# Kernel tuning notes

Measured on AMD Instinct MI355X. Metric: run time of the kernel, lower is better.

The kernel has to match this reference:

```python
import jax, jax.numpy as jnp
import numpy as np

N_NODES = 100000
N_EDGES = 1600000
D_IN = 128
D_HID = 128
D_OUT = 1


def setup_inputs() -> dict:
    key = jax.random.key(0)
    ks = jax.random.split(key, 8)
    x = jax.random.normal(ks[0], (N_NODES, D_IN), dtype=jnp.float32)
    edge_index = jax.random.randint(ks[1], (2, N_EDGES), 0, N_NODES, dtype=jnp.int64)
    s1 = 1.0 / np.sqrt(D_IN)
    s2 = 1.0 / np.sqrt(D_HID)
    W1 = jax.random.uniform(ks[2], (D_IN, D_HID), jnp.float32, -s1, s1)
    b1 = jnp.zeros((D_HID,), jnp.float32)
    W2 = jax.random.uniform(ks[3], (D_HID, D_HID), jnp.float32, -s2, s2)
    b2 = jnp.zeros((D_HID,), jnp.float32)
    Wl = jax.random.uniform(ks[4], (D_HID, D_OUT), jnp.float32, -s2, s2)
    bl = jax.random.uniform(ks[5], (D_OUT,), jnp.float32, -s2, s2)
    return {"x": x, "edge_index": edge_index, "W1": W1, "b1": b1,
            "W2": W2, "b2": b2, "Wl": Wl, "bl": bl}


def _gcn_norm(edge_index, num_nodes):
    # Add self-loops, compute symmetric normalization 1/sqrt(deg_s * deg_d).
    loops = jnp.arange(num_nodes, dtype=edge_index.dtype)
    src = jnp.concatenate([edge_index[0], loops])
    dst = jnp.concatenate([edge_index[1], loops])
    deg = jax.ops.segment_sum(jnp.ones_like(dst, dtype=jnp.float32), dst,
                              num_segments=num_nodes)
    dinv = jnp.where(deg > 0, jax.lax.rsqrt(deg), 0.0)
    norm = dinv[src] * dinv[dst]  # [E + N]
    return src, dst, norm


def _gcn_conv(h, W, b, src, dst, norm, num_nodes):
    h = h @ W                                  # [N, d_out]
    msg = h[src] * norm[:, None]               # [E+N, d_out] gather
    out = jax.ops.segment_sum(msg, dst, num_segments=num_nodes)  # scatter-add
    return out + b


def reference(x, edge_index, W1, b1, W2, b2, Wl, bl):
    num_nodes = x.shape[0]
    src, dst, norm = _gcn_norm(edge_index, num_nodes)
    h = jax.nn.relu(_gcn_conv(x, W1, b1, src, dst, norm, num_nodes))
    # dropout is identity in eval mode
    h = jax.nn.relu(_gcn_conv(h, W2, b2, src, dst, norm, num_nodes))
    return h @ Wl + bl
```

## Files before the change

kernel.cpp:

```cpp
#include <hip/hip_runtime.h>

#define DHID 128
#define BCAP 10240
#define PCHUNK 4096
#define XS_LD 136
#define SMEM_BYTES 21504

typedef _Float16 h4 __attribute__((ext_vector_type(4)));
typedef _Float16 h8 __attribute__((ext_vector_type(8)));
typedef float    f32x4 __attribute__((ext_vector_type(4)));

__device__ inline void hoist_afrag_f16(const _Float16* __restrict__ Wt, int w, int l16, int lq,
                                       h8 afrag[2][4]) {
#pragma unroll
    for (int ct = 0; ct < 2; ++ct) {
        int c = w * 32 + ct * 16 + l16;
#pragma unroll
        for (int kb = 0; kb < 4; ++kb)
            afrag[ct][kb] = *(const h8*)(Wt + (size_t)c * DHID + kb * 32 + lq * 8);
    }
}

__global__ __launch_bounds__(256) void k_prep(const float* __restrict__ W1,
                                              const float* __restrict__ W2,
                                              _Float16* __restrict__ W1t,
                                              _Float16* __restrict__ W2t) {
    const float* W = (blockIdx.x == 0) ? W1 : W2;
    _Float16* Wt   = (blockIdx.x == 0) ? W1t : W2t;
    int t = threadIdx.x;
    int c = t & 127, k0 = (t >> 7) * 64;
#pragma unroll
    for (int kb = 0; kb < 8; ++kb) {
        h8 v;
#pragma unroll
        for (int j = 0; j < 8; ++j)
            v[j] = (_Float16)W[(size_t)(k0 + kb * 8 + j) * DHID + c];
        *(h8*)(Wt + (size_t)c * DHID + k0 + kb * 8) = v;
    }
}

__device__ inline void gemm1_body(char* smem, const float* __restrict__ X,
                                  const _Float16* __restrict__ W1t,
                                  _Float16* __restrict__ Th, int N, int blk) {
    _Float16* Xs = (_Float16*)smem;
    int t = threadIdx.x;
    int w = t >> 6, l = t & 63, l16 = l & 15, lq = l >> 4;

    h8 afrag[2][4];
    hoist_afrag_f16(W1t, w, l16, lq, afrag);

    int rs = t >> 2, cs = (t & 3) * 32;
    int r0 = blk * 64;
    {
        int rg = r0 + rs; if (rg > N - 1) rg = N - 1;
        _Float16* sp = Xs + rs * XS_LD + cs;
        const float* xp = X + (size_t)rg * DHID + cs;
#pragma unroll
        for (int k = 0; k < 4; ++k) {
            float4 a = *(const float4*)(xp + k * 8);
            float4 b = *(const float4*)(xp + k * 8 + 4);
            h8 v;
            v[0] = (_Float16)a.x; v[1] = (_Float16)a.y;
            v[2] = (_Float16)a.z; v[3] = (_Float16)a.w;
            v[4] = (_Float16)b.x; v[5] = (_Float16)b.y;
            v[6] = (_Float16)b.z; v[7] = (_Float16)b.w;
            *(h8*)(sp + k * 8) = v;
        }
    }
    __syncthreads();

    f32x4 acc[4][2];
#pragma unroll
    for (int rt = 0; rt < 4; ++rt)
#pragma unroll
        for (int ct = 0; ct < 2; ++ct) acc[rt][ct] = (f32x4){0.f, 0.f, 0.f, 0.f};

#pragma unroll
    for (int rt = 0; rt < 4; ++rt) {
        const _Float16* bp = Xs + (rt * 16 + l16) * XS_LD + lq * 8;
#pragma unroll
        for (int kb = 0; kb < 4; ++kb) {
            h8 b = *(const h8*)(bp + kb * 32);
            acc[rt][0] = __builtin_amdgcn_mfma_f32_16x16x32_f16(afrag[0][kb], b, acc[rt][0], 0, 0, 0);
            acc[rt][1] = __builtin_amdgcn_mfma_f32_16x16x32_f16(afrag[1][kb], b, acc[rt][1], 0, 0, 0);
        }
    }

#pragma unroll
    for (int rt = 0; rt < 4; ++rt) {
        int r = r0 + rt * 16 + l16;
        if (r < N) {
#pragma unroll
            for (int ct = 0; ct < 2; ++ct) {
                h4 v;
#pragma unroll
                for (int j = 0; j < 4; ++j) v[j] = (_Float16)acc[rt][ct][j];
                *(h4*)(Th + (size_t)r * DHID + w * 32 + ct * 16 + lq * 4) = v;
            }
        }
    }
}

__device__ inline void partition_body(char* smem, const int* __restrict__ ei, int E, int nbuck,
                                      int* __restrict__ bcur, unsigned* __restrict__ packed, int blk) {
    unsigned* sdata = (unsigned*)smem;
    int* lcnt  = (int*)(smem + 16384);
    int* lbase = (int*)(smem + 17408);
    int* loff  = (int*)(smem + 18432);
    int* lcur  = (int*)(smem + 19456);
    int* sscan = (int*)(smem + 20480);
    int t = threadIdx.x;
    int e0 = blk * PCHUNK;
    lcnt[t] = 0;
    __syncthreads();

    int sreg[16], dreg[16];
#pragma unroll
    for (int k = 0; k < 16; ++k) {
        int e = e0 + t + k * 256;
        if (e < E) { sreg[k] = ei[e]; dreg[k] = ei[E + e]; }
        else dreg[k] = -1;
    }

#pragma unroll
    for (int k = 0; k < 16; ++k)
        if (dreg[k] >= 0) atomicAdd(&lcnt[dreg[k] >> 9], 1);
    __syncthreads();

    int c = lcnt[t];
    sscan[t] = c;
    __syncthreads();
    for (int off = 1; off < 256; off <<= 1) {
        int v = (t >= off) ? sscan[t - off] : 0;
        __syncthreads();
        sscan[t] += v;
        __syncthreads();
    }
    loff[t] = sscan[t] - c;
    if (t < nbuck && c > 0) lbase[t] = atomicAdd(&bcur[t], c);
    lcur[t] = sscan[t] - c;
    __syncthreads();

#pragma unroll
    for (int k = 0; k < 16; ++k) {
        if (dreg[k] >= 0) {
            int b = dreg[k] >> 9;
            int pos = atomicAdd(&lcur[b], 1);
            sdata[pos] = ((unsigned)(dreg[k] & 511) << 17) | (unsigned)sreg[k];
        }
    }
    __syncthreads();

    int wid = t >> 6, lane = t & 63;
    for (int b = wid; b < nbuck; b += 4) {
        int cb = lcnt[b];
        if (cb == 0) continue;
        int gbase = b * BCAP + lbase[b];
        int sbase = loff[b];
        for (int k = lane; k < cb; k += 64) packed[gbase + k] = sdata[sbase + k];
    }
}

__global__ __launch_bounds__(256) void k_front(const float* __restrict__ X,
                                               const _Float16* __restrict__ W1t,
                                               _Float16* __restrict__ Th, int N, int nRB,
                                               const int* __restrict__ ei, int E, int nbuck,
                                               int* __restrict__ bcur, unsigned* __restrict__ packed) {
    __shared__ __align__(16) char smem[SMEM_BYTES];
    if ((int)blockIdx.x < nRB)
        gemm1_body(smem, X, W1t, Th, N, blockIdx.x);
    else
        partition_body(smem, ei, E, nbuck, bcur, packed, blockIdx.x - nRB);
}

__global__ __launch_bounds__(256) void k_p2b(const unsigned* __restrict__ packed,
                                             const int* __restrict__ bcur,
                                             int* __restrict__ row_ptr,
                                             float* __restrict__ dinv,
                                             int* __restrict__ csr,
                                             int nbuck, int N, int E) {
    __shared__ int c512[512], cur512[512], sscan[256], sbk[256];
    int t = threadIdx.x, b = blockIdx.x;
    sbk[t] = (t < nbuck) ? bcur[t] : 0;
    c512[t] = 0; c512[t + 256] = 0;
    __syncthreads();
    for (int off = 1; off < 256; off <<= 1) {
        int v = (t >= off) ? sbk[t - off] : 0;
        __syncthreads();
        sbk[t] += v;
        __syncthreads();
    }
    int rbase = (b > 0) ? sbk[b - 1] : 0;
    int m = bcur[b];
    const unsigned* pb = packed + (size_t)b * BCAP;
    for (int i = t; i < m; i += 256) atomicAdd(&c512[pb[i] >> 17], 1);
    __syncthreads();
    int v0 = c512[2 * t], v1 = c512[2 * t + 1];
    int ps = v0 + v1;
    sscan[t] = ps;
    __syncthreads();
    for (int off = 1; off < 256; off <<= 1) {
        int v = (t >= off) ? sscan[t - off] : 0;
        __syncthreads();
        sscan[t] += v;
        __syncthreads();
    }
    int excl = sscan[t] - ps;
    cur512[2 * t] = excl;
    cur512[2 * t + 1] = excl + v0;

    int n0 = (b << 9) + 2 * t;
    if (n0 < N) {
        row_ptr[n0] = rbase + excl;
        dinv[n0] = rsqrtf((float)(v0 + 1));
    }
    if (n0 + 1 < N) {
        row_ptr[n0 + 1] = rbase + excl + v0;
        dinv[n0 + 1] = rsqrtf((float)(v1 + 1));
    }
    if (b == 0 && t == 0) row_ptr[N] = E;
    __syncthreads();

    for (int i = t; i < m; i += 256) {
        unsigned p = pb[i];
        int dl = p >> 17;
        int src = (int)(p & 0x1FFFFu);
        int pos = atomicAdd(&cur512[dl], 1);
        csr[rbase + pos] = src;
    }
}

__global__ __launch_bounds__(256) void k_agg_mid(const _Float16* __restrict__ Th,
                                                 const int* __restrict__ row_ptr,
                                                 const int* __restrict__ csr,
                                                 const float* __restrict__ dinv,
                                                 const float* __restrict__ bias,
                                                 _Float16* __restrict__ H, int N) {
    int node = blockIdx.x * 16 + (threadIdx.x >> 4);
    int sl = threadIdx.x & 15;
    if (node >= N) return;

    int e = row_ptr[node];
    int end = row_ptr[node + 1];
    const h8* Tl = (const h8*)Th + sl;

    float acc[8];
#pragma unroll
    for (int c = 0; c < 8; ++c) acc[c] = 0.f;

    for (; e + 4 <= end; e += 4) {
        int s0 = csr[e], s1 = csr[e + 1], s2 = csr[e + 2], s3 = csr[e + 3];
        float d0 = dinv[s0], d1 = dinv[s1], d2 = dinv[s2], d3 = dinv[s3];
        h8 v0 = Tl[(size_t)s0 * 16];
        h8 v1 = Tl[(size_t)s1 * 16];
        h8 v2 = Tl[(size_t)s2 * 16];
        h8 v3 = Tl[(size_t)s3 * 16];
#pragma unroll
        for (int c = 0; c < 8; ++c) {
            float a0 = fmaf(d0, (float)v0[c], fmaf(d1, (float)v1[c], 0.f));
            float a1 = fmaf(d2, (float)v2[c], fmaf(d3, (float)v3[c], 0.f));
            acc[c] += a0 + a1;
        }
    }
    for (; e < end; ++e) {
        int s0 = csr[e];
        float d0 = dinv[s0];
        h8 va = Tl[(size_t)s0 * 16];
#pragma unroll
        for (int c = 0; c < 8; ++c) acc[c] = fmaf(d0, (float)va[c], acc[c]);
    }

    float dn = dinv[node];
    {
        h8 tv = Tl[(size_t)node * 16];
#pragma unroll
        for (int c = 0; c < 8; ++c) acc[c] = fmaf(dn, (float)tv[c], acc[c]);
    }

    const float* bp = bias + sl * 8;
    float4 b0 = *(const float4*)bp;
    float4 b1 = *(const float4*)(bp + 4);
    h8 hv;
    hv[0] = (_Float16)fmaxf(fmaf(dn, acc[0], b0.x), 0.f);
    hv[1] = (_Float16)fmaxf(fmaf(dn, acc[1], b0.y), 0.f);
    hv[2] = (_Float16)fmaxf(fmaf(dn, acc[2], b0.z), 0.f);
    hv[3] = (_Float16)fmaxf(fmaf(dn, acc[3], b0.w), 0.f);
    hv[4] = (_Float16)fmaxf(fmaf(dn, acc[4], b1.x), 0.f);
    hv[5] = (_Float16)fmaxf(fmaf(dn, acc[5], b1.y), 0.f);
    hv[6] = (_Float16)fmaxf(fmaf(dn, acc[6], b1.z), 0.f);
    hv[7] = (_Float16)fmaxf(fmaf(dn, acc[7], b1.w), 0.f);
    *(h8*)(H + (size_t)node * DHID + sl * 8) = hv;
}

__global__ __launch_bounds__(256) void k_gemm_l2(const _Float16* __restrict__ H,
                                                 const _Float16* __restrict__ W2t,
                                                 _Float16* __restrict__ Th2, int N) {
    __shared__ _Float16 Xs[64 * XS_LD];
    int t = threadIdx.x;
    int w = t >> 6, l = t & 63, l16 = l & 15, lq = l >> 4;

    h8 afrag[2][4];
    hoist_afrag_f16(W2t, w, l16, lq, afrag);

    int rs = t >> 2, cs = (t & 3) * 32;
    int r0 = blockIdx.x * 64;
    {
        int rg = r0 + rs; if (rg > N - 1) rg = N - 1;
        _Float16* sp = Xs + rs * XS_LD + cs;
        const _Float16* xp = H + (size_t)rg * DHID + cs;
#pragma unroll
        for (int k = 0; k < 4; ++k)
            *(h8*)(sp + k * 8) = *(const h8*)(xp + k * 8);
    }
    __syncthreads();

    f32x4 acc[4][2];
#pragma unroll
    for (int rt = 0; rt < 4; ++rt)
#pragma unroll
        for (int ct = 0; ct < 2; ++ct) acc[rt][ct] = (f32x4){0.f, 0.f, 0.f, 0.f};

#pragma unroll
    for (int rt = 0; rt < 4; ++rt) {
        const _Float16* bp = Xs + (rt * 16 + l16) * XS_LD + lq * 8;
#pragma unroll
        for (int kb = 0; kb < 4; ++kb) {
            h8 b = *(const h8*)(bp + kb * 32);
            acc[rt][0] = __builtin_amdgcn_mfma_f32_16x16x32_f16(afrag[0][kb], b, acc[rt][0], 0, 0, 0);
            acc[rt][1] = __builtin_amdgcn_mfma_f32_16x16x32_f16(afrag[1][kb], b, acc[rt][1], 0, 0, 0);
        }
    }

#pragma unroll
    for (int rt = 0; rt < 4; ++rt) {
        int r = r0 + rt * 16 + l16;
        if (r < N) {
#pragma unroll
            for (int ct = 0; ct < 2; ++ct) {
                h4 v;
#pragma unroll
                for (int j = 0; j < 4; ++j) v[j] = (_Float16)acc[rt][ct][j];
                *(h4*)(Th2 + (size_t)r * DHID + w * 32 + ct * 16 + lq * 4) = v;
            }
        }
    }
}

__global__ __launch_bounds__(256) void k_agg_fin(const _Float16* __restrict__ Th2,
                                                 const int* __restrict__ row_ptr,
                                                 const int* __restrict__ csr,
                                                 const float* __restrict__ dinv,
                                                 const float* __restrict__ bias,
                                                 const float* __restrict__ Wl,
                                                 const float* __restrict__ bl,
                                                 float* __restrict__ out, int N) {
    int node = blockIdx.x * 16 + (threadIdx.x >> 4);
    int sl = threadIdx.x & 15;
    if (node >= N) return;

    int e = row_ptr[node];
    int end = row_ptr[node + 1];
    const h8* Tl = (const h8*)Th2 + sl;

    float acc[8];
#pragma unroll
    for (int c = 0; c < 8; ++c) acc[c] = 0.f;

    for (; e + 4 <= end; e += 4) {
        int s0 = csr[e], s1 = csr[e + 1], s2 = csr[e + 2], s3 = csr[e + 3];
        float d0 = dinv[s0], d1 = dinv[s1], d2 = dinv[s2], d3 = dinv[s3];
        h8 v0 = Tl[(size_t)s0 * 16];
        h8 v1 = Tl[(size_t)s1 * 16];
        h8 v2 = Tl[(size_t)s2 * 16];
        h8 v3 = Tl[(size_t)s3 * 16];
#pragma unroll
        for (int c = 0; c < 8; ++c) {
            float a0 = fmaf(d0, (float)v0[c], fmaf(d1, (float)v1[c], 0.f));
            float a1 = fmaf(d2, (float)v2[c], fmaf(d3, (float)v3[c], 0.f));
            acc[c] += a0 + a1;
        }
    }
    for (; e < end; ++e) {
        int s0 = csr[e];
        float d0 = dinv[s0];
        h8 va = Tl[(size_t)s0 * 16];
#pragma unroll
        for (int c = 0; c < 8; ++c) acc[c] = fmaf(d0, (float)va[c], acc[c]);
    }

    float dn = dinv[node];
    {
        h8 tv = Tl[(size_t)node * 16];
#pragma unroll
        for (int c = 0; c < 8; ++c) acc[c] = fmaf(dn, (float)tv[c], acc[c]);
    }

    const float* bp = bias + sl * 8;
    float4 b0 = *(const float4*)bp;
    float4 b1 = *(const float4*)(bp + 4);
    float r[8];
    r[0] = fmaxf(fmaf(dn, acc[0], b0.x), 0.f);
    r[1] = fmaxf(fmaf(dn, acc[1], b0.y), 0.f);
    r[2] = fmaxf(fmaf(dn, acc[2], b0.z), 0.f);
    r[3] = fmaxf(fmaf(dn, acc[3], b0.w), 0.f);
    r[4] = fmaxf(fmaf(dn, acc[4], b1.x), 0.f);
    r[5] = fmaxf(fmaf(dn, acc[5], b1.y), 0.f);
    r[6] = fmaxf(fmaf(dn, acc[6], b1.z), 0.f);
    r[7] = fmaxf(fmaf(dn, acc[7], b1.w), 0.f);

    const float* wp = Wl + sl * 8;
    float4 w0 = *(const float4*)wp;
    float4 w1 = *(const float4*)(wp + 4);
    float p = r[0] * w0.x + r[1] * w0.y + r[2] * w0.z + r[3] * w0.w +
              r[4] * w1.x + r[5] * w1.y + r[6] * w1.z + r[7] * w1.w;
#pragma unroll
    for (int off = 8; off > 0; off >>= 1) p += __shfl_down(p, off, 16);
    if (sl == 0) out[node] = p + bl[0];
}

extern "C" void kernel_launch(void* const* d_in, const int* in_sizes, int n_in,
                              void* d_out, int out_size, void* d_ws, size_t ws_size,
                              hipStream_t stream) {
    const float* x  = (const float*)d_in[0];
    const int*   ei = (const int*)d_in[1];
    const float* W1 = (const float*)d_in[2];
    const float* b1 = (const float*)d_in[3];
    const float* W2 = (const float*)d_in[4];
    const float* b2 = (const float*)d_in[5];
    const float* Wl = (const float*)d_in[6];
    const float* bl = (const float*)d_in[7];
    float* out = (float*)d_out;

    int N = in_sizes[0] / DHID;
    int E = in_sizes[1] / 2;
    int nbuck = (N + 511) / 512;
    int nRB = (N + 63) / 64;
    int nPart = (E + PCHUNK - 1) / PCHUNK;

    char* ws = (char*)d_ws;
    size_t off = 0;
    auto alloc = [&](size_t bytes) -> void* {
        void* p = ws + off;
        off += (bytes + 255) & ~(size_t)255;
        return p;
    };
    float*    dinv     = (float*)alloc((size_t)N * 4);
    int*      row_ptr  = (int*)alloc((size_t)(N + 1) * 4);
    int*      bcur     = (int*)alloc((size_t)nbuck * 4);
    int*      csr      = (int*)alloc((size_t)E * 4);
    unsigned* packed   = (unsigned*)alloc((size_t)nbuck * BCAP * 4);
    _Float16* Th       = (_Float16*)alloc((size_t)N * DHID * 2);
    _Float16* Th2      = (_Float16*)alloc((size_t)N * DHID * 2);
    _Float16* H        = (_Float16*)alloc((size_t)N * DHID * 2);
    _Float16* W1t      = (_Float16*)alloc((size_t)DHID * DHID * 2);
    _Float16* W2t      = (_Float16*)alloc((size_t)DHID * DHID * 2);

    (void)hipMemsetAsync(bcur, 0, (size_t)nbuck * 4, stream);

    k_prep<<<2, 256, 0, stream>>>(W1, W2, W1t, W2t);
    k_front<<<nRB + nPart, 256, 0, stream>>>(x, W1t, Th, N, nRB, ei, E, nbuck, bcur, packed);
    k_p2b<<<nbuck, 256, 0, stream>>>(packed, bcur, row_ptr, dinv, csr, nbuck, N, E);
    k_agg_mid<<<(N + 15) / 16, 256, 0, stream>>>(Th, row_ptr, csr, dinv, b1, H, N);
    k_gemm_l2<<<nRB, 256, 0, stream>>>(H, W2t, Th2, N);
    k_agg_fin<<<(N + 15) / 16, 256, 0, stream>>>(Th2, row_ptr, csr, dinv, b2, Wl, bl, out, N);
}
```

Before: 208.1 us.

## Regroup front kernels: merge weight prep into partition, GEMM1 into CSR build

Result: faster. 200.8 us (median of 2 runs) (-3.5%).

```diff
diff --git a/kernel.cpp b/kernel.cpp
--- a/kernel.cpp
+++ b/kernel.cpp
@@ -4,7 +4,8 @@
 #define BCAP 10240
 #define PCHUNK 4096
 #define XS_LD 136
-#define SMEM_BYTES 21504
+#define SMEM_PART 21504
+#define SMEM_MID  17408
 
 typedef _Float16 h4 __attribute__((ext_vector_type(4)));
 typedef _Float16 h8 __attribute__((ext_vector_type(8)));
@@ -21,12 +22,7 @@
     }
 }
 
-__global__ __launch_bounds__(256) void k_prep(const float* __restrict__ W1,
-                                              const float* __restrict__ W2,
-                                              _Float16* __restrict__ W1t,
-                                              _Float16* __restrict__ W2t) {
-    const float* W = (blockIdx.x == 0) ? W1 : W2;
-    _Float16* Wt   = (blockIdx.x == 0) ? W1t : W2t;
+__device__ inline void wtrans_body(const float* __restrict__ W, _Float16* __restrict__ Wt) {
     int t = threadIdx.x;
     int c = t & 127, k0 = (t >> 7) * 64;
 #pragma unroll
@@ -36,68 +32,6 @@
         for (int j = 0; j < 8; ++j)
             v[j] = (_Float16)W[(size_t)(k0 + kb * 8 + j) * DHID + c];
         *(h8*)(Wt + (size_t)c * DHID + k0 + kb * 8) = v;
-    }
-}
-
-__device__ inline void gemm1_body(char* smem, const float* __restrict__ X,
-                                  const _Float16* __restrict__ W1t,
-                                  _Float16* __restrict__ Th, int N, int blk) {
-    _Float16* Xs = (_Float16*)smem;
-    int t = threadIdx.x;
-    int w = t >> 6, l = t & 63, l16 = l & 15, lq = l >> 4;
-
-    h8 afrag[2][4];
-    hoist_afrag_f16(W1t, w, l16, lq, afrag);
-
-    int rs = t >> 2, cs = (t & 3) * 32;
-    int r0 = blk * 64;
-    {
-        int rg = r0 + rs; if (rg > N - 1) rg = N - 1;
-        _Float16* sp = Xs + rs * XS_LD + cs;
-        const float* xp = X + (size_t)rg * DHID + cs;
-#pragma unroll
-        for (int k = 0; k < 4; ++k) {
-            float4 a = *(const float4*)(xp + k * 8);
-            float4 b = *(const float4*)(xp + k * 8 + 4);
-            h8 v;
-            v[0] = (_Float16)a.x; v[1] = (_Float16)a.y;
-            v[2] = (_Float16)a.z; v[3] = (_Float16)a.w;
-            v[4] = (_Float16)b.x; v[5] = (_Float16)b.y;
-            v[6] = (_Float16)b.z; v[7] = (_Float16)b.w;
-            *(h8*)(sp + k * 8) = v;
-        }
-    }
-    __syncthreads();
-
-    f32x4 acc[4][2];
-#pragma unroll
-    for (int rt = 0; rt < 4; ++rt)
-#pragma unroll
-        for (int ct = 0; ct < 2; ++ct) acc[rt][ct] = (f32x4){0.f, 0.f, 0.f, 0.f};
-
-#pragma unroll
-    for (int rt = 0; rt < 4; ++rt) {
-        const _Float16* bp = Xs + (rt * 16 + l16) * XS_LD + lq * 8;
-#pragma unroll
-        for (int kb = 0; kb < 4; ++kb) {
-            h8 b = *(const h8*)(bp + kb * 32);
-            acc[rt][0] = __builtin_amdgcn_mfma_f32_16x16x32_f16(afrag[0][kb], b, acc[rt][0], 0, 0, 0);
-            acc[rt][1] = __builtin_amdgcn_mfma_f32_16x16x32_f16(afrag[1][kb], b, acc[rt][1], 0, 0, 0);
-        }
-    }
-
-#pragma unroll
-    for (int rt = 0; rt < 4; ++rt) {
-        int r = r0 + rt * 16 + l16;
-        if (r < N) {
-#pragma unroll
-            for (int ct = 0; ct < 2; ++ct) {
-                h4 v;
-#pragma unroll
-                for (int j = 0; j < 4; ++j) v[j] = (_Float16)acc[rt][ct][j];
-                *(h4*)(Th + (size_t)r * DHID + w * 32 + ct * 16 + lq * 4) = v;
-            }
-        }
     }
 }
 
@@ -161,26 +95,27 @@
     }
 }
 
-__global__ __launch_bounds__(256) void k_front(const float* __restrict__ X,
-                                               const _Float16* __restrict__ W1t,
-                                               _Float16* __restrict__ Th, int N, int nRB,
-                                               const int* __restrict__ ei, int E, int nbuck,
-                                               int* __restrict__ bcur, unsigned* __restrict__ packed) {
-    __shared__ __align__(16) char smem[SMEM_BYTES];
-    if ((int)blockIdx.x < nRB)
-        gemm1_body(smem, X, W1t, Th, N, blockIdx.x);
-    else
-        partition_body(smem, ei, E, nbuck, bcur, packed, blockIdx.x - nRB);
-}
-
-__global__ __launch_bounds__(256) void k_p2b(const unsigned* __restrict__ packed,
-                                             const int* __restrict__ bcur,
-                                             int* __restrict__ row_ptr,
-                                             float* __restrict__ dinv,
-                                             int* __restrict__ csr,
-                                             int nbuck, int N, int E) {
-    __shared__ int c512[512], cur512[512], sscan[256], sbk[256];
-    int t = threadIdx.x, b = blockIdx.x;
+__global__ __launch_bounds__(256) void k_part(const int* __restrict__ ei, int E, int nbuck,
+                                              int* __restrict__ bcur, unsigned* __restrict__ packed,
+                                              const float* __restrict__ W1, const float* __restrict__ W2,
+                                              _Float16* __restrict__ W1t, _Float16* __restrict__ W2t,
+                                              int nPart) {
+    __shared__ __align__(16) char smem[SMEM_PART];
+    int b = blockIdx.x;
+    if (b < nPart)            partition_body(smem, ei, E, nbuck, bcur, packed, b);
+    else if (b == nPart)      wtrans_body(W1, W1t);
+    else                      wtrans_body(W2, W2t);
+}
+
+__device__ inline void p2b_body(char* smem, const unsigned* __restrict__ packed,
+                                const int* __restrict__ bcur,
+                                int* __restrict__ row_ptr, float* __restrict__ dinv,
+                                int* __restrict__ csr, int nbuck, int N, int E, int b) {
+    int* c512   = (int*)smem;
+    int* cur512 = (int*)(smem + 2048);
+    int* sscan  = (int*)(smem + 4096);
+    int* sbk    = (int*)(smem + 5120);
+    int t = threadIdx.x;
     sbk[t] = (t < nbuck) ? bcur[t] : 0;
     c512[t] = 0; c512[t + 256] = 0;
     __syncthreads();
@@ -228,6 +163,83 @@
         int pos = atomicAdd(&cur512[dl], 1);
         csr[rbase + pos] = src;
     }
+}
+
+__device__ inline void gemm1_body(char* smem, const float* __restrict__ X,
+                                  const _Float16* __restrict__ W1t,
+                                  _Float16* __restrict__ Th, int N, int blk) {
+    _Float16* Xs = (_Float16*)smem;
+    int t = threadIdx.x;
+    int w = t >> 6, l = t & 63, l16 = l & 15, lq = l >> 4;
+
+    h8 afrag[2][4];
+    hoist_afrag_f16(W1t, w, l16, lq, afrag);
+
+    int rs = t >> 2, cs = (t & 3) * 32;
+    int r0 = blk * 64;
+    {
+        int rg = r0 + rs; if (rg > N - 1) rg = N - 1;
+        _Float16* sp = Xs + rs * XS_LD + cs;
+        const float* xp = X + (size_t)rg * DHID + cs;
+#pragma unroll
+        for (int k = 0; k < 4; ++k) {
+            float4 a = *(const float4*)(xp + k * 8);
+            float4 b = *(const float4*)(xp + k * 8 + 4);
+            h8 v;
+            v[0] = (_Float16)a.x; v[1] = (_Float16)a.y;
+            v[2] = (_Float16)a.z; v[3] = (_Float16)a.w;
+            v[4] = (_Float16)b.x; v[5] = (_Float16)b.y;
+            v[6] = (_Float16)b.z; v[7] = (_Float16)b.w;
+            *(h8*)(sp + k * 8) = v;
+        }
+    }
+    __syncthreads();
+
+    f32x4 acc[4][2];
+#pragma unroll
+    for (int rt = 0; rt < 4; ++rt)
+#pragma unroll
+        for (int ct = 0; ct < 2; ++ct) acc[rt][ct] = (f32x4){0.f, 0.f, 0.f, 0.f};
+
+#pragma unroll
+    for (int rt = 0; rt < 4; ++rt) {
+        const _Float16* bp = Xs + (rt * 16 + l16) * XS_LD + lq * 8;
+#pragma unroll
+        for (int kb = 0; kb < 4; ++kb) {
+            h8 b = *(const h8*)(bp + kb * 32);
+            acc[rt][0] = __builtin_amdgcn_mfma_f32_16x16x32_f16(afrag[0][kb], b, acc[rt][0], 0, 0, 0);
+            acc[rt][1] = __builtin_amdgcn_mfma_f32_16x16x32_f16(afrag[1][kb], b, acc[rt][1], 0, 0, 0);
+        }
+    }
+
+#pragma unroll
+    for (int rt = 0; rt < 4; ++rt) {
+        int r = r0 + rt * 16 + l16;
+        if (r < N) {
+#pragma unroll
+            for (int ct = 0; ct < 2; ++ct) {
+                h4 v;
+#pragma unroll
+                for (int j = 0; j < 4; ++j) v[j] = (_Float16)acc[rt][ct][j];
+                *(h4*)(Th + (size_t)r * DHID + w * 32 + ct * 16 + lq * 4) = v;
+            }
+        }
+    }
+}
+
+__global__ __launch_bounds__(256) void k_mid(const unsigned* __restrict__ packed,
+                                             const int* __restrict__ bcur,
+                                             int* __restrict__ row_ptr, float* __restrict__ dinv,
+                                             int* __restrict__ csr, int nbuck, int N, int E,
+                                             const float* __restrict__ X,
+                                             const _Float16* __restrict__ W1t,
+                                             _Float16* __restrict__ Th) {
+    __shared__ __align__(16) char smem[SMEM_MID];
+    int b = blockIdx.x;
+    if (b < nbuck)
+        p2b_body(smem, packed, bcur, row_ptr, dinv, csr, nbuck, N, E, b);
+    else
+        gemm1_body(smem, X, W1t, Th, N, b - nbuck);
 }
 
 __global__ __launch_bounds__(256) void k_agg_mid(const _Float16* __restrict__ Th,
@@ -457,9 +469,9 @@
 
     (void)hipMemsetAsync(bcur, 0, (size_t)nbuck * 4, stream);
 
-    k_prep<<<2, 256, 0, stream>>>(W1, W2, W1t, W2t);
-    k_front<<<nRB + nPart, 256, 0, stream>>>(x, W1t, Th, N, nRB, ei, E, nbuck, bcur, packed);
-    k_p2b<<<nbuck, 256, 0, stream>>>(packed, bcur, row_ptr, dinv, csr, nbuck, N, E);
+    k_part<<<nPart + 2, 256, 0, stream>>>(ei, E, nbuck, bcur, packed, W1, W2, W1t, W2t, nPart);
+    k_mid<<<nbuck + nRB, 256, 0, stream>>>(packed, bcur, row_ptr, dinv, csr, nbuck, N, E,
+                                           x, W1t, Th);
     k_agg_mid<<<(N + 15) / 16, 256, 0, stream>>>(Th, row_ptr, csr, dinv, b1, H, N);
     k_gemm_l2<<<nRB, 256, 0, stream>>>(H, W2t, Th2, N);
     k_agg_fin<<<(N + 15) / 16, 256, 0, stream>>>(Th2, row_ptr, csr, dinv, b2, Wl, bl, out, N);
```
